# Performance work log

Hardware: AMD Instinct MI355X
Metric: run time of the kernel (lower is better)

The kernel has to match this reference:

```python
import jax, jax.numpy as jnp
import numpy as np

N = 67108864          # total nodes across all graphs
B = 16384             # number of graphs (segments)

def setup_inputs() -> dict:
    key = jax.random.key(0)
    kx, ks = jax.random.split(key)
    x = jax.random.normal(kx, (N,), dtype=jnp.float32)
    # sorted segment ids <=> ragged torch.split(x, graph_size_list)
    segment_ids = jnp.sort(jax.random.randint(ks, (N,), 0, B, dtype=jnp.int32))
    return {"x": x, "segment_ids": segment_ids, "num_segments": B}

def reference(x, segment_ids, num_segments):
    # per-segment numerically-stable softmax (fused scatter_softmax form)
    seg_max = jax.ops.segment_max(x, segment_ids, num_segments=num_segments)
    e = jnp.exp(x - seg_max[segment_ids])
    seg_sum = jax.ops.segment_sum(e, segment_ids, num_segments=num_segments)
    return e / seg_sum[segment_ids]
```

## Files before the change

kernel.cpp:

```cpp
#include <hip/hip_runtime.h>
#include <hip/hip_bf16.h>
#include <float.h>


#define BLOCK 256
#define NWAVES (BLOCK / 64)

__global__ void seg_bounds_kernel(const int* __restrict__ ids, int n, int B,
                                  int* __restrict__ bounds) {
    int b = blockIdx.x * blockDim.x + threadIdx.x;
    if (b > B) return;
    if (b == B) { bounds[B] = n; return; }
    int lo = 0, hi = n;
    while (lo < hi) {
        int mid = (lo + hi) >> 1;
        if (ids[mid] < b) lo = mid + 1; else hi = mid;
    }
    bounds[b] = lo;
}

__device__ inline void sm_combine(float& m, float& l, float m2, float l2) {
    float M = fmaxf(m, m2);
    l = l * __expf(m - M) + l2 * __expf(m2 - M);
    m = M;
}

__global__ __launch_bounds__(BLOCK) void seg_softmax_kernel(
        const float* __restrict__ x, const int* __restrict__ bounds,
        float* __restrict__ out) {
    const int s = blockIdx.x;
    const int start = bounds[s];
    const int end   = bounds[s + 1];
    const int len   = end - start;
    if (len <= 0) return;

    const int tid = threadIdx.x;

    float m = -FLT_MAX;
    float l = 0.0f;
    for (int i = start + tid; i < end; i += BLOCK) {
        float v = x[i];
        float nm = fmaxf(m, v);
        l = l * __expf(m - nm) + __expf(v - nm);
        m = nm;
    }

    #pragma unroll
    for (int off = 32; off > 0; off >>= 1) {
        float m2 = __shfl_xor(m, off, 64);
        float l2 = __shfl_xor(l, off, 64);
        sm_combine(m, l, m2, l2);
    }

    __shared__ float sm[NWAVES], sl[NWAVES];
    const int wave = tid >> 6;
    const int lane = tid & 63;
    if (lane == 0) { sm[wave] = m; sl[wave] = l; }
    __syncthreads();

    float M = sm[0];
    float L = sl[0];
    #pragma unroll
    for (int w = 1; w < NWAVES; w++) {
        sm_combine(M, L, sm[w], sl[w]);
    }
    const float invL = 1.0f / L;

    for (int i = start + tid; i < end; i += BLOCK) {
        out[i] = __expf(x[i] - M) * invL;
    }
}

extern "C" void kernel_launch(void* const* d_in, const int* in_sizes, int n_in,
                              void* d_out, int out_size, void* d_ws, size_t ws_size,
                              hipStream_t stream) {
    const float* x   = (const float*)d_in[0];
    const int*   ids = (const int*)d_in[1];
    const int N = in_sizes[0];
    const int B = 16384;

    int* bounds = (int*)d_ws;

    {
        int threads = 256;
        int blocks = (B + 1 + threads - 1) / threads;
        seg_bounds_kernel<<<blocks, threads, 0, stream>>>(ids, N, B, bounds);
    }
    {
        seg_softmax_kernel<<<B, BLOCK, 0, stream>>>(x, bounds, (float*)d_out);
    }
}
```

Baseline: 626.1 us.

## Cache segment in registers with float4 loads and two-pass max/sum softmax

Each block now loads its segment once as aligned float4 vectors into a per-thread register cache (up to 6 float4 per thread), with scalar head and tail handling. The max and the sum are computed in separate passes, replacing the online rescaling, and the exponentials are reused for the output, so x is not re-read from global memory. This is meant to cut global read traffic, exp count and per-element instruction overhead. It adds an extra block barrier and raises register pressure. Segments longer than the cache fall back to re-reading x.

```diff
diff --git a/kernel.cpp b/kernel.cpp
--- a/kernel.cpp
+++ b/kernel.cpp
@@ -1,10 +1,10 @@
 #include <hip/hip_runtime.h>
-#include <hip/hip_bf16.h>
 #include <float.h>
 
 
 #define BLOCK 256
 #define NWAVES (BLOCK / 64)
+#define VEC_CAP 6
 
 __global__ void seg_bounds_kernel(const int* __restrict__ ids, int n, int B,
                                   int* __restrict__ bounds) {
@@ -19,10 +19,18 @@
     bounds[b] = lo;
 }
 
-__device__ inline void sm_combine(float& m, float& l, float m2, float l2) {
-    float M = fmaxf(m, m2);
-    l = l * __expf(m - M) + l2 * __expf(m2 - M);
-    m = M;
+__device__ inline float wave_max(float v) {
+    #pragma unroll
+    for (int off = 32; off > 0; off >>= 1)
+        v = fmaxf(v, __shfl_xor(v, off, 64));
+    return v;
+}
+
+__device__ inline float wave_sum(float v) {
+    #pragma unroll
+    for (int off = 32; off > 0; off >>= 1)
+        v += __shfl_xor(v, off, 64);
+    return v;
 }
 
 __global__ __launch_bounds__(BLOCK) void seg_softmax_kernel(
@@ -31,43 +39,93 @@
     const int s = blockIdx.x;
     const int start = bounds[s];
     const int end   = bounds[s + 1];
-    const int len   = end - start;
-    if (len <= 0) return;
+    if (end <= start) return;
 
-    const int tid = threadIdx.x;
+    const int tid  = threadIdx.x;
+    const int wave = tid >> 6;
+    const int lane = tid & 63;
 
+    int a0 = (start + 3) & ~3;
+    if (a0 > end) a0 = end;
+    const int a1    = a0 + ((end - a0) & ~3);
+    const int headn = a0 - start;
+    const int tailn = end - a1;
+    const int nvec  = (a1 - a0) >> 2;
+    const float4* __restrict__ xv = (const float4*)x + (a0 >> 2);
+    float4*       __restrict__ ov = (float4*)out + (a0 >> 2);
+
+    float4 xc[VEC_CAP];
+    float hx = 0.0f, tx = 0.0f;
     float m = -FLT_MAX;
-    float l = 0.0f;
-    for (int i = start + tid; i < end; i += BLOCK) {
-        float v = x[i];
-        float nm = fmaxf(m, v);
-        l = l * __expf(m - nm) + __expf(v - nm);
-        m = nm;
+    if (tid < headn) { hx = x[start + tid]; m = fmaxf(m, hx); }
+    if (tid < tailn) { tx = x[a1 + tid];    m = fmaxf(m, tx); }
+    #pragma unroll
+    for (int iv = 0; iv < VEC_CAP; ++iv) {
+        const int idx = tid + iv * BLOCK;
+        if (idx < nvec) {
+            const float4 v = xv[idx];
+            xc[iv] = v;
+            m = fmaxf(fmaxf(m, fmaxf(v.x, v.y)), fmaxf(v.z, v.w));
+        }
     }
-
-    #pragma unroll
-    for (int off = 32; off > 0; off >>= 1) {
-        float m2 = __shfl_xor(m, off, 64);
-        float l2 = __shfl_xor(l, off, 64);
-        sm_combine(m, l, m2, l2);
+    for (int idx = tid + VEC_CAP * BLOCK; idx < nvec; idx += BLOCK) {
+        const float4 v = xv[idx];
+        m = fmaxf(fmaxf(m, fmaxf(v.x, v.y)), fmaxf(v.z, v.w));
     }
 
     __shared__ float sm[NWAVES], sl[NWAVES];
-    const int wave = tid >> 6;
-    const int lane = tid & 63;
-    if (lane == 0) { sm[wave] = m; sl[wave] = l; }
+    m = wave_max(m);
+    if (lane == 0) sm[wave] = m;
     __syncthreads();
+    float M = sm[0];
+    #pragma unroll
+    for (int w = 1; w < NWAVES; ++w) M = fmaxf(M, sm[w]);
 
-    float M = sm[0];
+    float l = 0.0f;
+    if (tid < headn) { hx = __expf(hx - M); l += hx; }
+    if (tid < tailn) { tx = __expf(tx - M); l += tx; }
+    #pragma unroll
+    for (int iv = 0; iv < VEC_CAP; ++iv) {
+        const int idx = tid + iv * BLOCK;
+        if (idx < nvec) {
+            float4 v = xc[iv];
+            v.x = __expf(v.x - M); v.y = __expf(v.y - M);
+            v.z = __expf(v.z - M); v.w = __expf(v.w - M);
+            xc[iv] = v;
+            l += (v.x + v.y) + (v.z + v.w);
+        }
+    }
+    for (int idx = tid + VEC_CAP * BLOCK; idx < nvec; idx += BLOCK) {
+        const float4 v = xv[idx];
+        l += __expf(v.x - M) + __expf(v.y - M) +
+             __expf(v.z - M) + __expf(v.w - M);
+    }
+
+    l = wave_sum(l);
+    if (lane == 0) sl[wave] = l;
+    __syncthreads();
     float L = sl[0];
     #pragma unroll
-    for (int w = 1; w < NWAVES; w++) {
-        sm_combine(M, L, sm[w], sl[w]);
-    }
+    for (int w = 1; w < NWAVES; ++w) L += sl[w];
     const float invL = 1.0f / L;
 
-    for (int i = start + tid; i < end; i += BLOCK) {
-        out[i] = __expf(x[i] - M) * invL;
+    if (tid < headn) out[start + tid] = hx * invL;
+    if (tid < tailn) out[a1 + tid]    = tx * invL;
+    #pragma unroll
+    for (int iv = 0; iv < VEC_CAP; ++iv) {
+        const int idx = tid + iv * BLOCK;
+        if (idx < nvec) {
+            float4 v = xc[iv];
+            v.x *= invL; v.y *= invL; v.z *= invL; v.w *= invL;
+            ov[idx] = v;
+        }
+    }
+    for (int idx = tid + VEC_CAP * BLOCK; idx < nvec; idx += BLOCK) {
+        const float4 v = xv[idx];
+        float4 w;
+        w.x = __expf(v.x - M) * invL; w.y = __expf(v.y - M) * invL;
+        w.z = __expf(v.z - M) * invL; w.w = __expf(v.w - M) * invL;
+        ov[idx] = w;
     }
 }
 
```

Measured after the change: 550.3 us. -12.1%, faster.
